# Kernel optimization log

Hardware: AMD Instinct MI355X
Metric: run time of the kernel (lower is better)

The kernel has to match this reference:

```python
import jax, jax.numpy as jnp
import numpy as np

N_NODES = 50000
N_EDGES = 800000
IN_DIM = 128
HID_DIM = 128
N_CLASSES = 64


def gcn_conv(x, edge_index, W, b):
    """PyG GCNConv: add self-loops, sym deg^-1/2 norm, xW, scatter-add, +bias."""
    n = x.shape[0]
    loop = jnp.arange(n, dtype=edge_index.dtype)
    src = jnp.concatenate([edge_index[0], loop])  # [E+N]
    dst = jnp.concatenate([edge_index[1], loop])  # [E+N]
    ones = jnp.ones(src.shape[0], dtype=x.dtype)
    deg = jax.ops.segment_sum(ones, dst, num_segments=n)  # in-degree incl self-loop
    dinv = jnp.where(deg > 0, jax.lax.rsqrt(deg), jnp.zeros_like(deg))
    norm = dinv[src] * dinv[dst]  # [E+N]
    h = x @ W  # [N, out]
    msg = h[src] * norm[:, None]  # [E+N, out] gather + scale
    out = jax.ops.segment_sum(msg, dst, num_segments=n)  # scatter-add
    return out + b


def setup_inputs() -> dict:
    key = jax.random.key(0)
    k1, k2, k3, k4, k5 = jax.random.split(key, 5)
    x = jax.random.normal(k1, (N_NODES, IN_DIM), dtype=jnp.float32)
    edge_index = jax.random.randint(k2, (2, N_EDGES), 0, N_NODES, dtype=jnp.int64)
    # Glorot-style init for the two GCNConv linear weights; zero biases (PyG default)
    s1 = 1.0 / np.sqrt(IN_DIM)
    s2 = 1.0 / np.sqrt(HID_DIM)
    W1 = jax.random.uniform(k3, (IN_DIM, HID_DIM), jnp.float32, -s1, s1)
    b1 = jnp.zeros((HID_DIM,), jnp.float32)
    W2 = jax.random.uniform(k4, (HID_DIM, N_CLASSES), jnp.float32, -s2, s2)
    b2 = jnp.zeros((N_CLASSES,), jnp.float32)
    return {"x": x, "edge_index": edge_index, "W1": W1, "b1": b1, "W2": W2, "b2": b2}


def reference(x, edge_index, W1, b1, W2, b2):
    h = gcn_conv(x, edge_index, W1, b1)
    h = jax.nn.relu(h)
    out = gcn_conv(h, edge_index, W2, b2)
    return out
```

## Files before the change

kernel.cpp:

```cpp
#include <hip/hip_runtime.h>
#include <hip/hip_bf16.h>
#include <hip/hip_fp16.h>


#define CHUNK 4096
#define BSHIFT 7
#define BSIZE 128
#define BCAP 4096

typedef unsigned int uint;
typedef _Float16 f16x8 __attribute__((ext_vector_type(8)));
typedef float f32x4 __attribute__((ext_vector_type(4)));

__device__ __forceinline__ float2 h2f(uint v) {
  __half2 h;
  __builtin_memcpy(&h, &v, 4);
  return __half22float2(h);
}

__device__ __forceinline__ uint f2h(float a, float b) {
  __half2 h = __halves2half2(__float2half_rn(a), __float2half_rn(b));
  uint r;
  __builtin_memcpy(&r, &h, 4);
  return r;
}

__device__ __forceinline__ int block_is64(const int* ei, int* s_is64) {
  if (threadIdx.x < 64) {
    unsigned long long m = __ballot(ei[2 * threadIdx.x + 1] != 0);
    if (threadIdx.x == 0) *s_is64 = (m == 0ULL) ? 1 : 0;
  }
  __syncthreads();
  return *s_is64;
}

__global__ void prep_k(const float* __restrict__ W1,
                       const float* __restrict__ W2,
                       _Float16* __restrict__ P,
                       int* __restrict__ totals, int nbuck) {
  int li = blockIdx.x * 256 + threadIdx.x;
  if (li < nbuck) totals[li] = 0;
  if (li >= 24576) return;
  const float* W;
  _Float16* dst;
  int NC, idx;
  if (li < 16384) { W = W1; dst = P;         NC = 128; idx = li; }
  else            { W = W2; dst = P + 16384; NC = 64;  idx = li - 16384; }
  int NF = NC >> 4;
  int j = idx & 7;
  int l = (idx >> 3) & 63;
  int rest = idx >> 9;
  int c = rest % NF;
  int t = rest / NF;
  int k = t * 32 + ((l >> 4) << 3) + j;
  int col = c * 16 + (l & 15);
  dst[idx] = (_Float16)W[(size_t)k * NC + col];
}

template <int NC, bool A16>
__device__ __forceinline__ void gemm_body(const void* __restrict__ Xv,
                                          const _Float16* __restrict__ Wp,
                                          _Float16* __restrict__ H,
                                          int M, int blk) {
  constexpr int NF = NC / 16;
  int lane = threadIdx.x & 63;
  int w = threadIdx.x >> 6;
  int row0 = blk * 64 + w * 16;
  int arow = row0 + (lane & 15);
  bool av = arow < M;
  const uint4* wp = (const uint4*)Wp;

  f32x4 acc[NF];
#pragma unroll
  for (int c = 0; c < NF; ++c) acc[c] = (f32x4){0.f, 0.f, 0.f, 0.f};

#pragma unroll
  for (int t = 0; t < 4; ++t) {
    f16x8 a;
    if constexpr (A16) {
      const _Float16* xr = (const _Float16*)Xv + (size_t)arow * 128 + ((lane >> 4) << 3);
      uint4 araw = av ? *(const uint4*)(xr + t * 32) : make_uint4(0u, 0u, 0u, 0u);
      __builtin_memcpy(&a, &araw, 16);
    } else {
      const float* xr = (const float*)Xv + (size_t)arow * 128 + ((lane >> 4) << 3);
      float4 lo = av ? *(const float4*)(xr + t * 32) : make_float4(0.f, 0.f, 0.f, 0.f);
      float4 hi = av ? *(const float4*)(xr + t * 32 + 4) : make_float4(0.f, 0.f, 0.f, 0.f);
      a[0] = (_Float16)lo.x; a[1] = (_Float16)lo.y;
      a[2] = (_Float16)lo.z; a[3] = (_Float16)lo.w;
      a[4] = (_Float16)hi.x; a[5] = (_Float16)hi.y;
      a[6] = (_Float16)hi.z; a[7] = (_Float16)hi.w;
    }
#pragma unroll
    for (int c = 0; c < NF; ++c) {
      uint4 braw = wp[(t * NF + c) * 64 + lane];
      f16x8 b;
      __builtin_memcpy(&b, &braw, 16);
      acc[c] = __builtin_amdgcn_mfma_f32_16x16x32_f16(a, b, acc[c], 0, 0, 0);
    }
  }

  int rbase = row0 + ((lane >> 4) << 2);
#pragma unroll
  for (int r = 0; r < 4; ++r) {
    int row = rbase + r;
    if (row < M) {
#pragma unroll
      for (int c = 0; c < NF; ++c)
        H[(size_t)row * NC + c * 16 + (lane & 15)] = (_Float16)acc[c][r];
    }
  }
}

__global__ __launch_bounds__(256) void gemm1_hist_k(const float* __restrict__ x,
                                                    const _Float16* __restrict__ pW1,
                                                    _Float16* __restrict__ h1,
                                                    const int* __restrict__ ei,
                                                    int* __restrict__ gh,
                                                    int* __restrict__ totals,
                                                    int M, int E, int GB,
                                                    int nchunk, int nbuck) {
  if ((int)blockIdx.x < GB) {
    gemm_body<128, false>(x, pW1, h1, M, blockIdx.x);
    return;
  }
  __shared__ int h[512];
  __shared__ int s_is64;
  int c = blockIdx.x - GB;
  for (int i = threadIdx.x; i < 512; i += 256) h[i] = 0;
  int is64 = block_is64(ei, &s_is64);
  int base = c * CHUNK;
  int lim = min(CHUNK, E - base);
  for (int i = threadIdx.x; i < lim; i += 256) {
    int e = base + i;
    int d = is64 ? ei[2 * ((size_t)E + e)] : ei[(size_t)E + e];
    atomicAdd(&h[d >> BSHIFT], 1);
  }
  __syncthreads();
  for (int k = threadIdx.x; k < nbuck; k += 256) {
    gh[k * nchunk + c] = h[k];
    atomicAdd(&totals[k], h[k]);
  }
}

__global__ __launch_bounds__(256) void scanrow_k(const int* __restrict__ gh,
                                                 const int* __restrict__ totals,
                                                 int* __restrict__ gbase,
                                                 int* __restrict__ bucketStart,
                                                 int* __restrict__ offsets,
                                                 int nchunk, int nbuck, int N, int E) {
  __shared__ int st[256];
  int k = blockIdx.x;
  int t = threadIdx.x;
  int partial = 0;
  for (int i = t; i < k; i += 256) partial += totals[i];
  st[t] = partial;
  __syncthreads();
  for (int o = 128; o > 0; o >>= 1) {
    if (t < o) st[t] += st[t + o];
    __syncthreads();
  }
  int bs = st[0];
  if (t == 0) {
    bucketStart[k] = bs;
    if (k == nbuck - 1) { bucketStart[nbuck] = E; offsets[N] = E; }
  }
  __syncthreads();
  int x = (t < nchunk) ? gh[k * nchunk + t] : 0;
  st[t] = x;
  __syncthreads();
  int incl = x;
  for (int o = 1; o < 256; o <<= 1) {
    int add = (t >= o) ? st[t - o] : 0;
    __syncthreads();
    incl += add;
    st[t] = incl;
    __syncthreads();
  }
  if (t < nchunk) gbase[k * nchunk + t] = bs + (incl - x);
}

__global__ __launch_bounds__(256) void part_k(const int* __restrict__ ei,
                                              const int* __restrict__ gbase,
                                              int* __restrict__ tmp,
                                              int E, int nchunk, int nbuck) {
  __shared__ int cur[512];
  __shared__ int s_is64;
  int c = blockIdx.x;
  for (int i = threadIdx.x; i < nbuck; i += 256) cur[i] = gbase[i * nchunk + c];
  int is64 = block_is64(ei, &s_is64);
  int base = c * CHUNK;
  int lim = min(CHUNK, E - base);
  for (int i = threadIdx.x; i < lim; i += 256) {
    int e = base + i;
    int s, d;
    if (is64) {
      s = ei[2 * (size_t)e];
      d = ei[2 * ((size_t)E + e)];
    } else {
      s = ei[e];
      d = ei[(size_t)E + e];
    }
    int p = atomicAdd(&cur[d >> BSHIFT], 1);
    tmp[p] = s | ((d & (BSIZE - 1)) << 16);
  }
}

__global__ __launch_bounds__(256) void bucket_k(const int* __restrict__ tmp,
                                                const int* __restrict__ bucketStart,
                                                int* __restrict__ csr_src,
                                                int* __restrict__ offsets,
                                                float* __restrict__ dinv,
                                                int N) {
  __shared__ int ebuf[BCAP];
  __shared__ int cnt[BSIZE];
  __shared__ int st[256];
  __shared__ int lofs[BSIZE];
  int k = blockIdx.x;
  int b0 = bucketStart[k], b1 = bucketStart[k + 1];
  int sz = b1 - b0;
  int t = threadIdx.x;
  if (t < BSIZE) cnt[t] = 0;
  __syncthreads();
  bool inlds = (sz <= BCAP);
  if (inlds) {
    for (int i = t; i < sz; i += 256) {
      int v = tmp[b0 + i];
      ebuf[i] = v;
      atomicAdd(&cnt[v >> 16], 1);
    }
  } else {
    for (int i = t; i < sz; i += 256) atomicAdd(&cnt[tmp[b0 + i] >> 16], 1);
  }
  __syncthreads();
  int x = (t < BSIZE) ? cnt[t] : 0;
  st[t] = x;
  __syncthreads();
  int incl = x;
  for (int o = 1; o < 256; o <<= 1) {
    int add = (t >= o) ? st[t - o] : 0;
    __syncthreads();
    incl += add;
    st[t] = incl;
    __syncthreads();
  }
  int node = (k << BSHIFT) + t;
  if (t < BSIZE) {
    lofs[t] = incl - x;
    if (node < N) {
      offsets[node] = b0 + lofs[t];
      dinv[node] = rsqrtf((float)(x + 1));
    }
  }
  __syncthreads();
  if (t < BSIZE) cnt[t] = lofs[t];
  __syncthreads();
  if (inlds) {
    for (int i = t; i < sz; i += 256) {
      int v = ebuf[i];
      int p = atomicAdd(&cnt[v >> 16], 1);
      csr_src[b0 + p] = v & 0xFFFF;
    }
  } else {
    for (int i = t; i < sz; i += 256) {
      int v = tmp[b0 + i];
      int p = atomicAdd(&cnt[v >> 16], 1);
      csr_src[b0 + p] = v & 0xFFFF;
    }
  }
}

__global__ __launch_bounds__(256) void gemm2_k(const _Float16* __restrict__ y,
                                               const _Float16* __restrict__ pW2,
                                               _Float16* __restrict__ h2, int M) {
  gemm_body<64, true>(y, pW2, h2, M, blockIdx.x);
}

__global__ __launch_bounds__(256) void agg1_k(const uint2* __restrict__ hp,
                                              const float* __restrict__ dinv,
                                              const int* __restrict__ offsets,
                                              const int* __restrict__ csr_src,
                                              const float* __restrict__ b,
                                              uint2* __restrict__ y, int n) {
  int wv = threadIdx.x >> 6;
  int lane = threadIdx.x & 63;
  int half = lane >> 5;
  int fl = lane & 31;
  int node = blockIdx.x * 8 + wv * 2 + half;
  if (node >= n) return;
  int beg = offsets[node], end = offsets[node + 1];
  int deg = end - beg;
  float di = dinv[node];
  uint2 su = hp[(size_t)node * 32 + fl];
  float2 sl = h2f(su.x), sh = h2f(su.y);
  float a0 = di * sl.x, a1 = di * sl.y, a2 = di * sh.x, a3 = di * sh.y;
  int sv = 0;
  float dv = 0.f;
  if (fl < deg) { sv = csr_src[beg + fl]; dv = dinv[sv]; }
  int lim = deg < 32 ? deg : 32;
  int e = 0;
  for (; e + 8 <= lim; e += 8) {
    int sA = __shfl(sv, e + 0, 32), sB = __shfl(sv, e + 1, 32);
    int sC = __shfl(sv, e + 2, 32), sD = __shfl(sv, e + 3, 32);
    int sE = __shfl(sv, e + 4, 32), sF = __shfl(sv, e + 5, 32);
    int sG = __shfl(sv, e + 6, 32), sH = __shfl(sv, e + 7, 32);
    float dA = __shfl(dv, e + 0, 32), dB = __shfl(dv, e + 1, 32);
    float dC = __shfl(dv, e + 2, 32), dD = __shfl(dv, e + 3, 32);
    float dE = __shfl(dv, e + 4, 32), dF = __shfl(dv, e + 5, 32);
    float dG = __shfl(dv, e + 6, 32), dH = __shfl(dv, e + 7, 32);
    uint2 uA = hp[(size_t)sA * 32 + fl];
    uint2 uB = hp[(size_t)sB * 32 + fl];
    uint2 uC = hp[(size_t)sC * 32 + fl];
    uint2 uD = hp[(size_t)sD * 32 + fl];
    uint2 uE = hp[(size_t)sE * 32 + fl];
    uint2 uF = hp[(size_t)sF * 32 + fl];
    uint2 uG = hp[(size_t)sG * 32 + fl];
    uint2 uH = hp[(size_t)sH * 32 + fl];
    float2 lA = h2f(uA.x), hA = h2f(uA.y), lB = h2f(uB.x), hB = h2f(uB.y);
    float2 lC = h2f(uC.x), hC = h2f(uC.y), lD = h2f(uD.x), hD = h2f(uD.y);
    float2 lE = h2f(uE.x), hE = h2f(uE.y), lF = h2f(uF.x), hF = h2f(uF.y);
    float2 lG = h2f(uG.x), hG = h2f(uG.y), lH = h2f(uH.x), hH = h2f(uH.y);
    a0 = fmaf(dA, lA.x, a0); a1 = fmaf(dA, lA.y, a1);
    a2 = fmaf(dA, hA.x, a2); a3 = fmaf(dA, hA.y, a3);
    a0 = fmaf(dB, lB.x, a0); a1 = fmaf(dB, lB.y, a1);
    a2 = fmaf(dB, hB.x, a2); a3 = fmaf(dB, hB.y, a3);
    a0 = fmaf(dC, lC.x, a0); a1 = fmaf(dC, lC.y, a1);
    a2 = fmaf(dC, hC.x, a2); a3 = fmaf(dC, hC.y, a3);
    a0 = fmaf(dD, lD.x, a0); a1 = fmaf(dD, lD.y, a1);
    a2 = fmaf(dD, hD.x, a2); a3 = fmaf(dD, hD.y, a3);
    a0 = fmaf(dE, lE.x, a0); a1 = fmaf(dE, lE.y, a1);
    a2 = fmaf(dE, hE.x, a2); a3 = fmaf(dE, hE.y, a3);
    a0 = fmaf(dF, lF.x, a0); a1 = fmaf(dF, lF.y, a1);
    a2 = fmaf(dF, hF.x, a2); a3 = fmaf(dF, hF.y, a3);
    a0 = fmaf(dG, lG.x, a0); a1 = fmaf(dG, lG.y, a1);
    a2 = fmaf(dG, hG.x, a2); a3 = fmaf(dG, hG.y, a3);
    a0 = fmaf(dH, lH.x, a0); a1 = fmaf(dH, lH.y, a1);
    a2 = fmaf(dH, hH.x, a2); a3 = fmaf(dH, hH.y, a3);
  }
  for (; e < lim; ++e) {
    int s = __shfl(sv, e, 32);
    float dd = __shfl(dv, e, 32);
    uint2 u = hp[(size_t)s * 32 + fl];
    float2 l = h2f(u.x), h = h2f(u.y);
    a0 = fmaf(dd, l.x, a0); a1 = fmaf(dd, l.y, a1);
    a2 = fmaf(dd, h.x, a2); a3 = fmaf(dd, h.y, a3);
  }
  for (int ee = beg + 32; ee < end; ++ee) {
    int s = csr_src[ee];
    float dd = dinv[s];
    uint2 u = hp[(size_t)s * 32 + fl];
    float2 l = h2f(u.x), h = h2f(u.y);
    a0 = fmaf(dd, l.x, a0); a1 = fmaf(dd, l.y, a1);
    a2 = fmaf(dd, h.x, a2); a3 = fmaf(dd, h.y, a3);
  }
  float4 bb = *(const float4*)(b + 4 * fl);
  float o0 = fmaxf(fmaf(di, a0, bb.x), 0.f);
  float o1 = fmaxf(fmaf(di, a1, bb.y), 0.f);
  float o2 = fmaxf(fmaf(di, a2, bb.z), 0.f);
  float o3 = fmaxf(fmaf(di, a3, bb.w), 0.f);
  uint2 o;
  o.x = f2h(o0, o1);
  o.y = f2h(o2, o3);
  y[(size_t)node * 32 + fl] = o;
}

__global__ __launch_bounds__(256) void agg2_k(const uint* __restrict__ hp,
                                              const float* __restrict__ dinv,
                                              const int* __restrict__ offsets,
                                              const int* __restrict__ csr_src,
                                              const float* __restrict__ b,
                                              float* __restrict__ out, int n) {
  int wv = threadIdx.x >> 6;
  int lane = threadIdx.x & 63;
  int half = lane >> 5;
  int fl = lane & 31;
  int node = blockIdx.x * 8 + wv * 2 + half;
  if (node >= n) return;
  int beg = offsets[node], end = offsets[node + 1];
  int deg = end - beg;
  float di = dinv[node];
  float2 self = h2f(hp[(size_t)node * 32 + fl]);
  float ax = di * self.x, ay = di * self.y;
  int sv = 0;
  float dv = 0.f;
  if (fl < deg) { sv = csr_src[beg + fl]; dv = dinv[sv]; }
  int lim = deg < 32 ? deg : 32;
  int e = 0;
  for (; e + 8 <= lim; e += 8) {
    int s0 = __shfl(sv, e + 0, 32), s1 = __shfl(sv, e + 1, 32);
    int s2 = __shfl(sv, e + 2, 32), s3 = __shfl(sv, e + 3, 32);
    int s4 = __shfl(sv, e + 4, 32), s5 = __shfl(sv, e + 5, 32);
    int s6 = __shfl(sv, e + 6, 32), s7 = __shfl(sv, e + 7, 32);
    float d0 = __shfl(dv, e + 0, 32), d1 = __shfl(dv, e + 1, 32);
    float d2 = __shfl(dv, e + 2, 32), d3 = __shfl(dv, e + 3, 32);
    float d4 = __shfl(dv, e + 4, 32), d5 = __shfl(dv, e + 5, 32);
    float d6 = __shfl(dv, e + 6, 32), d7 = __shfl(dv, e + 7, 32);
    uint u0 = hp[(size_t)s0 * 32 + fl];
    uint u1 = hp[(size_t)s1 * 32 + fl];
    uint u2 = hp[(size_t)s2 * 32 + fl];
    uint u3 = hp[(size_t)s3 * 32 + fl];
    uint u4 = hp[(size_t)s4 * 32 + fl];
    uint u5 = hp[(size_t)s5 * 32 + fl];
    uint u6 = hp[(size_t)s6 * 32 + fl];
    uint u7 = hp[(size_t)s7 * 32 + fl];
    float2 v0 = h2f(u0), v1 = h2f(u1), v2 = h2f(u2), v3 = h2f(u3);
    float2 v4 = h2f(u4), v5 = h2f(u5), v6 = h2f(u6), v7 = h2f(u7);
    ax = fmaf(d0, v0.x, ax); ay = fmaf(d0, v0.y, ay);
    ax = fmaf(d1, v1.x, ax); ay = fmaf(d1, v1.y, ay);
    ax = fmaf(d2, v2.x, ax); ay = fmaf(d2, v2.y, ay);
    ax = fmaf(d3, v3.x, ax); ay = fmaf(d3, v3.y, ay);
    ax = fmaf(d4, v4.x, ax); ay = fmaf(d4, v4.y, ay);
    ax = fmaf(d5, v5.x, ax); ay = fmaf(d5, v5.y, ay);
    ax = fmaf(d6, v6.x, ax); ay = fmaf(d6, v6.y, ay);
    ax = fmaf(d7, v7.x, ax); ay = fmaf(d7, v7.y, ay);
  }
  for (; e < lim; ++e) {
    int s = __shfl(sv, e, 32);
    float dd = __shfl(dv, e, 32);
    float2 v = h2f(hp[(size_t)s * 32 + fl]);
    ax = fmaf(dd, v.x, ax);
    ay = fmaf(dd, v.y, ay);
  }
  for (int ee = beg + 32; ee < end; ++ee) {
    int s = csr_src[ee];
    float dd = dinv[s];
    float2 v = h2f(hp[(size_t)s * 32 + fl]);
    ax = fmaf(dd, v.x, ax);
    ay = fmaf(dd, v.y, ay);
  }
  float2 bb = ((const float2*)b)[fl];
  float2 o;
  o.x = fmaf(di, ax, bb.x);
  o.y = fmaf(di, ay, bb.y);
  ((float2*)out)[(size_t)node * 32 + fl] = o;
}

extern "C" void kernel_launch(void* const* d_in, const int* in_sizes, int n_in,
                              void* d_out, int out_size, void* d_ws, size_t ws_size,
                              hipStream_t stream) {
  const float* x  = (const float*)d_in[0];
  const int*   ei = (const int*)d_in[1];
  const float* W1 = (const float*)d_in[2];
  const float* b1 = (const float*)d_in[3];
  const float* W2 = (const float*)d_in[4];
  const float* b2 = (const float*)d_in[5];
  float* out = (float*)d_out;

  const int N = in_sizes[0] / 128;
  const int E = in_sizes[1] / 2;
  const int NBUCK = (N + BSIZE - 1) >> BSHIFT;
  const int NCHUNK = (E + CHUNK - 1) / CHUNK;

  char* w = (char*)d_ws;
  size_t off = 0;
  auto alloc = [&](size_t bytes) -> void* {
    void* p = w + off;
    off = (off + bytes + 511) & ~(size_t)511;
    return p;
  };
  int*       gh      = (int*)alloc((size_t)NBUCK * NCHUNK * 4);
  int*       gbase   = (int*)alloc((size_t)NBUCK * NCHUNK * 4);
  int*       totals  = (int*)alloc((size_t)NBUCK * 4);
  int*       bstart  = (int*)alloc((size_t)(NBUCK + 1) * 4);
  int*       tmp     = (int*)alloc((size_t)E * 4);
  int*       offsets = (int*)alloc((size_t)(N + 1) * 4);
  float*     dinv    = (float*)alloc((size_t)N * 4);
  int*       csr_src = (int*)alloc((size_t)E * 4);
  _Float16*  pW      = (_Float16*)alloc(24576 * 2);
  _Float16*  h1      = (_Float16*)alloc((size_t)N * 128 * 2);
  _Float16*  y       = (_Float16*)alloc((size_t)N * 128 * 2);
  _Float16*  h2      = (_Float16*)alloc((size_t)N * 64 * 2);

  const int GB = (N + 63) / 64;
  const int AB = (N + 7) / 8;

  prep_k<<<96, 256, 0, stream>>>(W1, W2, pW, totals, NBUCK);
  gemm1_hist_k<<<GB + NCHUNK, 256, 0, stream>>>(x, pW, h1, ei, gh, totals,
                                                N, E, GB, NCHUNK, NBUCK);
  scanrow_k<<<NBUCK, 256, 0, stream>>>(gh, totals, gbase, bstart, offsets,
                                       NCHUNK, NBUCK, N, E);
  part_k<<<NCHUNK, 256, 0, stream>>>(ei, gbase, tmp, E, NCHUNK, NBUCK);
  bucket_k<<<NBUCK, 256, 0, stream>>>(tmp, bstart, csr_src, offsets, dinv, N);

  agg1_k<<<AB, 256, 0, stream>>>((const uint2*)h1, dinv, offsets, csr_src, b1,
                                 (uint2*)y, N);
  gemm2_k<<<GB, 256, 0, stream>>>(y, pW + 16384, h2, N);
  agg2_k<<<AB, 256, 0, stream>>>((const uint*)h2, dinv, offsets, csr_src, b2, out, N);
}
```

Baseline: 107.5 us.

## Fuse layer-1 aggregation with layer-2 GEMM through shared memory

Merges the first aggregation kernel and the second GEMM into one kernel. Each block aggregates 64 nodes into an LDS tile and then runs MFMA against W2 directly from LDS. This removes the fp16 intermediate y round-trip through global memory and one kernel launch. In exchange, each block now processes 8 aggregation iterations serially with far fewer blocks (GB instead of AB), which reduces parallelism for the latency-bound gather and adds LDS usage and a block barrier.

```diff
diff --git a/kernel.cpp b/kernel.cpp
--- a/kernel.cpp
+++ b/kernel.cpp
@@ -57,11 +57,11 @@
   dst[idx] = (_Float16)W[(size_t)k * NC + col];
 }
 
-template <int NC, bool A16>
-__device__ __forceinline__ void gemm_body(const void* __restrict__ Xv,
-                                          const _Float16* __restrict__ Wp,
-                                          _Float16* __restrict__ H,
-                                          int M, int blk) {
+template <int NC>
+__device__ __forceinline__ void gemm_body_f32A(const float* __restrict__ X,
+                                               const _Float16* __restrict__ Wp,
+                                               _Float16* __restrict__ H,
+                                               int M, int blk) {
   constexpr int NF = NC / 16;
   int lane = threadIdx.x & 63;
   int w = threadIdx.x >> 6;
@@ -76,20 +76,14 @@
 
 #pragma unroll
   for (int t = 0; t < 4; ++t) {
+    const float* xr = X + (size_t)arow * 128 + ((lane >> 4) << 3);
+    float4 lo = av ? *(const float4*)(xr + t * 32) : make_float4(0.f, 0.f, 0.f, 0.f);
+    float4 hi = av ? *(const float4*)(xr + t * 32 + 4) : make_float4(0.f, 0.f, 0.f, 0.f);
     f16x8 a;
-    if constexpr (A16) {
-      const _Float16* xr = (const _Float16*)Xv + (size_t)arow * 128 + ((lane >> 4) << 3);
-      uint4 araw = av ? *(const uint4*)(xr + t * 32) : make_uint4(0u, 0u, 0u, 0u);
-      __builtin_memcpy(&a, &araw, 16);
-    } else {
-      const float* xr = (const float*)Xv + (size_t)arow * 128 + ((lane >> 4) << 3);
-      float4 lo = av ? *(const float4*)(xr + t * 32) : make_float4(0.f, 0.f, 0.f, 0.f);
-      float4 hi = av ? *(const float4*)(xr + t * 32 + 4) : make_float4(0.f, 0.f, 0.f, 0.f);
-      a[0] = (_Float16)lo.x; a[1] = (_Float16)lo.y;
-      a[2] = (_Float16)lo.z; a[3] = (_Float16)lo.w;
-      a[4] = (_Float16)hi.x; a[5] = (_Float16)hi.y;
-      a[6] = (_Float16)hi.z; a[7] = (_Float16)hi.w;
-    }
+    a[0] = (_Float16)lo.x; a[1] = (_Float16)lo.y;
+    a[2] = (_Float16)lo.z; a[3] = (_Float16)lo.w;
+    a[4] = (_Float16)hi.x; a[5] = (_Float16)hi.y;
+    a[6] = (_Float16)hi.z; a[7] = (_Float16)hi.w;
 #pragma unroll
     for (int c = 0; c < NF; ++c) {
       uint4 braw = wp[(t * NF + c) * 64 + lane];
@@ -120,7 +114,7 @@
                                                     int M, int E, int GB,
                                                     int nchunk, int nbuck) {
   if ((int)blockIdx.x < GB) {
-    gemm_body<128, false>(x, pW1, h1, M, blockIdx.x);
+    gemm_body_f32A<128>(x, pW1, h1, M, blockIdx.x);
     return;
   }
   __shared__ int h[512];
@@ -269,98 +263,132 @@
   }
 }
 
-__global__ __launch_bounds__(256) void gemm2_k(const _Float16* __restrict__ y,
-                                               const _Float16* __restrict__ pW2,
-                                               _Float16* __restrict__ h2, int M) {
-  gemm_body<64, true>(y, pW2, h2, M, blockIdx.x);
-}
-
-__global__ __launch_bounds__(256) void agg1_k(const uint2* __restrict__ hp,
-                                              const float* __restrict__ dinv,
-                                              const int* __restrict__ offsets,
-                                              const int* __restrict__ csr_src,
-                                              const float* __restrict__ b,
-                                              uint2* __restrict__ y, int n) {
+__global__ __launch_bounds__(256) void agg1_gemm2_k(const uint2* __restrict__ hp,
+                                                    const float* __restrict__ dinv,
+                                                    const int* __restrict__ offsets,
+                                                    const int* __restrict__ csr_src,
+                                                    const float* __restrict__ b,
+                                                    const _Float16* __restrict__ pW2,
+                                                    _Float16* __restrict__ h2, int n) {
+  __shared__ _Float16 ylds[64][136];
   int wv = threadIdx.x >> 6;
   int lane = threadIdx.x & 63;
   int half = lane >> 5;
   int fl = lane & 31;
-  int node = blockIdx.x * 8 + wv * 2 + half;
-  if (node >= n) return;
-  int beg = offsets[node], end = offsets[node + 1];
-  int deg = end - beg;
-  float di = dinv[node];
-  uint2 su = hp[(size_t)node * 32 + fl];
-  float2 sl = h2f(su.x), sh = h2f(su.y);
-  float a0 = di * sl.x, a1 = di * sl.y, a2 = di * sh.x, a3 = di * sh.y;
-  int sv = 0;
-  float dv = 0.f;
-  if (fl < deg) { sv = csr_src[beg + fl]; dv = dinv[sv]; }
-  int lim = deg < 32 ? deg : 32;
-  int e = 0;
-  for (; e + 8 <= lim; e += 8) {
-    int sA = __shfl(sv, e + 0, 32), sB = __shfl(sv, e + 1, 32);
-    int sC = __shfl(sv, e + 2, 32), sD = __shfl(sv, e + 3, 32);
-    int sE = __shfl(sv, e + 4, 32), sF = __shfl(sv, e + 5, 32);
-    int sG = __shfl(sv, e + 6, 32), sH = __shfl(sv, e + 7, 32);
-    float dA = __shfl(dv, e + 0, 32), dB = __shfl(dv, e + 1, 32);
-    float dC = __shfl(dv, e + 2, 32), dD = __shfl(dv, e + 3, 32);
-    float dE = __shfl(dv, e + 4, 32), dF = __shfl(dv, e + 5, 32);
-    float dG = __shfl(dv, e + 6, 32), dH = __shfl(dv, e + 7, 32);
-    uint2 uA = hp[(size_t)sA * 32 + fl];
-    uint2 uB = hp[(size_t)sB * 32 + fl];
-    uint2 uC = hp[(size_t)sC * 32 + fl];
-    uint2 uD = hp[(size_t)sD * 32 + fl];
-    uint2 uE = hp[(size_t)sE * 32 + fl];
-    uint2 uF = hp[(size_t)sF * 32 + fl];
-    uint2 uG = hp[(size_t)sG * 32 + fl];
-    uint2 uH = hp[(size_t)sH * 32 + fl];
-    float2 lA = h2f(uA.x), hA = h2f(uA.y), lB = h2f(uB.x), hB = h2f(uB.y);
-    float2 lC = h2f(uC.x), hC = h2f(uC.y), lD = h2f(uD.x), hD = h2f(uD.y);
-    float2 lE = h2f(uE.x), hE = h2f(uE.y), lF = h2f(uF.x), hF = h2f(uF.y);
-    float2 lG = h2f(uG.x), hG = h2f(uG.y), lH = h2f(uH.x), hH = h2f(uH.y);
-    a0 = fmaf(dA, lA.x, a0); a1 = fmaf(dA, lA.y, a1);
-    a2 = fmaf(dA, hA.x, a2); a3 = fmaf(dA, hA.y, a3);
-    a0 = fmaf(dB, lB.x, a0); a1 = fmaf(dB, lB.y, a1);
-    a2 = fmaf(dB, hB.x, a2); a3 = fmaf(dB, hB.y, a3);
-    a0 = fmaf(dC, lC.x, a0); a1 = fmaf(dC, lC.y, a1);
-    a2 = fmaf(dC, hC.x, a2); a3 = fmaf(dC, hC.y, a3);
-    a0 = fmaf(dD, lD.x, a0); a1 = fmaf(dD, lD.y, a1);
-    a2 = fmaf(dD, hD.x, a2); a3 = fmaf(dD, hD.y, a3);
-    a0 = fmaf(dE, lE.x, a0); a1 = fmaf(dE, lE.y, a1);
-    a2 = fmaf(dE, hE.x, a2); a3 = fmaf(dE, hE.y, a3);
-    a0 = fmaf(dF, lF.x, a0); a1 = fmaf(dF, lF.y, a1);
-    a2 = fmaf(dF, hF.x, a2); a3 = fmaf(dF, hF.y, a3);
-    a0 = fmaf(dG, lG.x, a0); a1 = fmaf(dG, lG.y, a1);
-    a2 = fmaf(dG, hG.x, a2); a3 = fmaf(dG, hG.y, a3);
-    a0 = fmaf(dH, lH.x, a0); a1 = fmaf(dH, lH.y, a1);
-    a2 = fmaf(dH, hH.x, a2); a3 = fmaf(dH, hH.y, a3);
-  }
-  for (; e < lim; ++e) {
-    int s = __shfl(sv, e, 32);
-    float dd = __shfl(dv, e, 32);
-    uint2 u = hp[(size_t)s * 32 + fl];
-    float2 l = h2f(u.x), h = h2f(u.y);
-    a0 = fmaf(dd, l.x, a0); a1 = fmaf(dd, l.y, a1);
-    a2 = fmaf(dd, h.x, a2); a3 = fmaf(dd, h.y, a3);
-  }
-  for (int ee = beg + 32; ee < end; ++ee) {
-    int s = csr_src[ee];
-    float dd = dinv[s];
-    uint2 u = hp[(size_t)s * 32 + fl];
-    float2 l = h2f(u.x), h = h2f(u.y);
-    a0 = fmaf(dd, l.x, a0); a1 = fmaf(dd, l.y, a1);
-    a2 = fmaf(dd, h.x, a2); a3 = fmaf(dd, h.y, a3);
-  }
-  float4 bb = *(const float4*)(b + 4 * fl);
-  float o0 = fmaxf(fmaf(di, a0, bb.x), 0.f);
-  float o1 = fmaxf(fmaf(di, a1, bb.y), 0.f);
-  float o2 = fmaxf(fmaf(di, a2, bb.z), 0.f);
-  float o3 = fmaxf(fmaf(di, a3, bb.w), 0.f);
-  uint2 o;
-  o.x = f2h(o0, o1);
-  o.y = f2h(o2, o3);
-  y[(size_t)node * 32 + fl] = o;
+  int base = blockIdx.x * 64;
+
+#pragma unroll 1
+  for (int iter = 0; iter < 8; ++iter) {
+    int lrow = iter * 8 + wv * 2 + half;
+    int node = base + lrow;
+    uint2 o = make_uint2(0u, 0u);
+    if (node < n) {
+      int beg = offsets[node], end = offsets[node + 1];
+      int deg = end - beg;
+      float di = dinv[node];
+      uint2 su = hp[(size_t)node * 32 + fl];
+      float2 sl = h2f(su.x), sh = h2f(su.y);
+      float a0 = di * sl.x, a1 = di * sl.y, a2 = di * sh.x, a3 = di * sh.y;
+      int sv = 0;
+      float dv = 0.f;
+      if (fl < deg) { sv = csr_src[beg + fl]; dv = dinv[sv]; }
+      int lim = deg < 32 ? deg : 32;
+      int e = 0;
+      for (; e + 8 <= lim; e += 8) {
+        int sA = __shfl(sv, e + 0, 32), sB = __shfl(sv, e + 1, 32);
+        int sC = __shfl(sv, e + 2, 32), sD = __shfl(sv, e + 3, 32);
+        int sE = __shfl(sv, e + 4, 32), sF = __shfl(sv, e + 5, 32);
+        int sG = __shfl(sv, e + 6, 32), sH = __shfl(sv, e + 7, 32);
+        float dA = __shfl(dv, e + 0, 32), dB = __shfl(dv, e + 1, 32);
+        float dC = __shfl(dv, e + 2, 32), dD = __shfl(dv, e + 3, 32);
+        float dE = __shfl(dv, e + 4, 32), dF = __shfl(dv, e + 5, 32);
+        float dG = __shfl(dv, e + 6, 32), dH = __shfl(dv, e + 7, 32);
+        uint2 uA = hp[(size_t)sA * 32 + fl];
+        uint2 uB = hp[(size_t)sB * 32 + fl];
+        uint2 uC = hp[(size_t)sC * 32 + fl];
+        uint2 uD = hp[(size_t)sD * 32 + fl];
+        uint2 uE = hp[(size_t)sE * 32 + fl];
+        uint2 uF = hp[(size_t)sF * 32 + fl];
+        uint2 uG = hp[(size_t)sG * 32 + fl];
+        uint2 uH = hp[(size_t)sH * 32 + fl];
+        float2 lA = h2f(uA.x), hA = h2f(uA.y), lB = h2f(uB.x), hB = h2f(uB.y);
+        float2 lC = h2f(uC.x), hC = h2f(uC.y), lD = h2f(uD.x), hD = h2f(uD.y);
+        float2 lE = h2f(uE.x), hE = h2f(uE.y), lF = h2f(uF.x), hF = h2f(uF.y);
+        float2 lG = h2f(uG.x), hG = h2f(uG.y), lH = h2f(uH.x), hH = h2f(uH.y);
+        a0 = fmaf(dA, lA.x, a0); a1 = fmaf(dA, lA.y, a1);
+        a2 = fmaf(dA, hA.x, a2); a3 = fmaf(dA, hA.y, a3);
+        a0 = fmaf(dB, lB.x, a0); a1 = fmaf(dB, lB.y, a1);
+        a2 = fmaf(dB, hB.x, a2); a3 = fmaf(dB, hB.y, a3);
+        a0 = fmaf(dC, lC.x, a0); a1 = fmaf(dC, lC.y, a1);
+        a2 = fmaf(dC, hC.x, a2); a3 = fmaf(dC, hC.y, a3);
+        a0 = fmaf(dD, lD.x, a0); a1 = fmaf(dD, lD.y, a1);
+        a2 = fmaf(dD, hD.x, a2); a3 = fmaf(dD, hD.y, a3);
+        a0 = fmaf(dE, lE.x, a0); a1 = fmaf(dE, lE.y, a1);
+        a2 = fmaf(dE, hE.x, a2); a3 = fmaf(dE, hE.y, a3);
+        a0 = fmaf(dF, lF.x, a0); a1 = fmaf(dF, lF.y, a1);
+        a2 = fmaf(dF, hF.x, a2); a3 = fmaf(dF, hF.y, a3);
+        a0 = fmaf(dG, lG.x, a0); a1 = fmaf(dG, lG.y, a1);
+        a2 = fmaf(dG, hG.x, a2); a3 = fmaf(dG, hG.y, a3);
+        a0 = fmaf(dH, lH.x, a0); a1 = fmaf(dH, lH.y, a1);
+        a2 = fmaf(dH, hH.x, a2); a3 = fmaf(dH, hH.y, a3);
+      }
+      for (; e < lim; ++e) {
+        int s = __shfl(sv, e, 32);
+        float dd = __shfl(dv, e, 32);
+        uint2 u = hp[(size_t)s * 32 + fl];
+        float2 l = h2f(u.x), h = h2f(u.y);
+        a0 = fmaf(dd, l.x, a0); a1 = fmaf(dd, l.y, a1);
+        a2 = fmaf(dd, h.x, a2); a3 = fmaf(dd, h.y, a3);
+      }
+      for (int ee = beg + 32; ee < end; ++ee) {
+        int s = csr_src[ee];
+        float dd = dinv[s];
+        uint2 u = hp[(size_t)s * 32 + fl];
+        float2 l = h2f(u.x), h = h2f(u.y);
+        a0 = fmaf(dd, l.x, a0); a1 = fmaf(dd, l.y, a1);
+        a2 = fmaf(dd, h.x, a2); a3 = fmaf(dd, h.y, a3);
+      }
+      float4 bb = *(const float4*)(b + 4 * fl);
+      float o0 = fmaxf(fmaf(di, a0, bb.x), 0.f);
+      float o1 = fmaxf(fmaf(di, a1, bb.y), 0.f);
+      float o2 = fmaxf(fmaf(di, a2, bb.z), 0.f);
+      float o3 = fmaxf(fmaf(di, a3, bb.w), 0.f);
+      o.x = f2h(o0, o1);
+      o.y = f2h(o2, o3);
+    }
+    *(uint2*)&ylds[lrow][fl * 4] = o;
+  }
+  __syncthreads();
+
+  constexpr int NF = 4;
+  const uint4* wp = (const uint4*)pW2;
+  int row0l = wv * 16;
+  f32x4 acc[NF];
+#pragma unroll
+  for (int c = 0; c < NF; ++c) acc[c] = (f32x4){0.f, 0.f, 0.f, 0.f};
+#pragma unroll
+  for (int t = 0; t < 4; ++t) {
+    f16x8 a;
+    uint4 araw = *(const uint4*)&ylds[row0l + (lane & 15)][t * 32 + ((lane >> 4) << 3)];
+    __builtin_memcpy(&a, &araw, 16);
+#pragma unroll
+    for (int c = 0; c < NF; ++c) {
+      uint4 braw = wp[(t * NF + c) * 64 + lane];
+      f16x8 bfrag;
+      __builtin_memcpy(&bfrag, &braw, 16);
+      acc[c] = __builtin_amdgcn_mfma_f32_16x16x32_f16(a, bfrag, acc[c], 0, 0, 0);
+    }
+  }
+  int rbase = row0l + ((lane >> 4) << 2);
+#pragma unroll
+  for (int r = 0; r < 4; ++r) {
+    int grow = base + rbase + r;
+    if (grow < n) {
+#pragma unroll
+      for (int c = 0; c < NF; ++c)
+        h2[(size_t)grow * 64 + c * 16 + (lane & 15)] = (_Float16)acc[c][r];
+    }
+  }
 }
 
 __global__ __launch_bounds__(256) void agg2_k(const uint* __restrict__ hp,
@@ -467,7 +495,6 @@
   int*       csr_src = (int*)alloc((size_t)E * 4);
   _Float16*  pW      = (_Float16*)alloc(24576 * 2);
   _Float16*  h1      = (_Float16*)alloc((size_t)N * 128 * 2);
-  _Float16*  y       = (_Float16*)alloc((size_t)N * 128 * 2);
   _Float16*  h2      = (_Float16*)alloc((size_t)N * 64 * 2);
 
   const int GB = (N + 63) / 64;
@@ -481,8 +508,7 @@
   part_k<<<NCHUNK, 256, 0, stream>>>(ei, gbase, tmp, E, NCHUNK, NBUCK);
   bucket_k<<<NBUCK, 256, 0, stream>>>(tmp, bstart, csr_src, offsets, dinv, N);
 
-  agg1_k<<<AB, 256, 0, stream>>>((const uint2*)h1, dinv, offsets, csr_src, b1,
-                                 (uint2*)y, N);
-  gemm2_k<<<GB, 256, 0, stream>>>(y, pW + 16384, h2, N);
+  agg1_gemm2_k<<<GB, 256, 0, stream>>>((const uint2*)h1, dinv, offsets, csr_src,
+                                       b1, pW + 16384, h2, N);
   agg2_k<<<AB, 256, 0, stream>>>((const uint*)h2, dinv, offsets, csr_src, b2, out, N);
 }
```

Result: slower. 113.4 us (+5.5%).
